# Performance work log

Measured on AMD Instinct MI355X. Metric: run time of the kernel, lower is better.

The kernel has to match this reference:

```python
import jax, jax.numpy as jnp
import numpy as np

T, H, W_, CIN, LAT, HID, OUT, NHL = 32, 64, 64, 3, 256, 256, 3, 3
OMEGA = 30.0  # SIREN sine frequency


def _uniform(key, shape, fan_in):
    b = np.sqrt(6.0 / fan_in) / OMEGA
    return jax.random.uniform(key, shape, jnp.float32, -b, b)


def setup_inputs() -> dict:
    key = jax.random.key(0)
    ks = jax.random.split(key, 10)
    return {
        "coords": jax.random.normal(ks[0], (T, H, W_, CIN), jnp.float32),
        "latents": jax.random.normal(ks[1], (T, LAT), jnp.float32),
        # shared SIREN weights (nf_net): W stored as (out, in) like nn.Linear
        "W0": _uniform(ks[2], (HID, CIN), CIN),
        "b0": jnp.zeros((HID,), jnp.float32),
        "Wh": _uniform(ks[3], (NHL, HID, HID), HID),
        "bh": jnp.zeros((NHL, HID), jnp.float32),
        "Wf": _uniform(ks[4], (OUT, HID), HID),
        "bf": jnp.zeros((OUT,), jnp.float32),
        # hypernet weight generators (hw_net), no bias
        "HW0": _uniform(ks[5], (HID * CIN, LAT), LAT),
        "HWh": _uniform(ks[6], (NHL, HID * HID, LAT), LAT),
        # hypernet bias generators (hb_net), no bias
        "HB": _uniform(ks[7], (NHL + 1, HID, LAT), LAT),
    }


def reference(coords, latents, W0, b0, Wh, bh, Wf, bf, HW0, HWh, HB):
    t = latents.shape[0]
    # per-frame hyper biases for all layers: (t, NHL+1, HID)
    hb = jnp.einsum('tl,khl->tkh', latents, HB)
    # layer 0: per-frame weight (t, HID, CIN)
    hw0 = (latents @ HW0.T).reshape(t, HID, CIN)
    x = coords  # (t,h,w,CIN)
    x = (x @ W0.T + b0
         + jnp.einsum('thwi,toi->thwo', x, hw0)
         + hb[:, 0][:, None, None, :])
    x = jnp.sin(OMEGA * x)
    for i in range(NHL):
        hw = (latents @ HWh[i].T).reshape(t, HID, HID)  # (t, HID, HID)
        x = (x @ Wh[i].T + bh[i]
             + jnp.einsum('thwi,toi->thwo', x, hw)
             + hb[:, i + 1][:, None, None, :])
        x = jnp.sin(OMEGA * x)
    return x @ Wf.T + bf  # (t,h,w,OUT)
```

## Files before the change

kernel.cpp:

```cpp
#include <hip/hip_runtime.h>
#include <cstdint>
#include <cstddef>

typedef __attribute__((ext_vector_type(8))) _Float16 f16x8;
typedef __attribute__((ext_vector_type(2))) __fp16 h2;
typedef __attribute__((ext_vector_type(16))) float f32x16;

#define LO_SCALE 2048.0f
#define LO_INV   (1.0f / 2048.0f)
#define OMEGA_SC 4.774648292756860f

union H8 { f16x8 v; _Float16 h[8]; };
union U2 { h2 v[2]; uint2 u; };

__global__ __launch_bounds__(256) void kab(
    const float* __restrict__ latents, const float* __restrict__ W0,
    const float* __restrict__ b0, const float* __restrict__ bh,
    const float* __restrict__ HW0, const float* __restrict__ HB,
    const float* __restrict__ Wh, const float* __restrict__ HWh,
    _Float16* __restrict__ w0blob, float* __restrict__ beff,
    _Float16* __restrict__ whblob) {
  __shared__ float lat_t[8192];
  int tid = threadIdx.x, bid = blockIdx.x;

  if (bid >= 768) {
    int id = (bid - 768) * 256 + tid;
    if (id < 32768) {
      int t = id >> 10, rem = id & 1023;
      int r2 = rem & 127, part = r2 >> 6, lane = r2 & 63;
      int nf = rem >> 7;
      int o = nf * 32 + (lane & 31), kc = lane >> 5;
      const float* lat = latents + t * 256;
      H8 outv;
#pragma unroll
      for (int j = 0; j < 8; ++j) outv.h[j] = (_Float16)0.0f;
#pragma unroll
      for (int j = 0; j < 8; ++j) {
        int i = kc * 8 + j;
        if (i < 3) {
          const float* row = HW0 + (o * 3 + i) * 256;
          float s = W0[o * 3 + i];
          for (int k = 0; k < 256; k += 4)
            s += row[k] * lat[k] + row[k + 1] * lat[k + 1] +
                 row[k + 2] * lat[k + 2] + row[k + 3] * lat[k + 3];
          s *= OMEGA_SC;
          _Float16 hi = (_Float16)s;
          outv.h[j] = part ? (_Float16)((s - (float)hi) * LO_SCALE) : hi;
        }
      }
      *(f16x8*)(w0blob + (size_t)id * 8) = outv.v;
    } else {
      int v = id - 32768;
      int t = v >> 10, k = (v >> 8) & 3, hm = v & 255;
      float base = (k == 0) ? b0[hm] : bh[(k - 1) * 256 + hm];
      const float* lat = latents + t * 256;
      const float* row = HB + (size_t)(k * 256 + hm) * 256;
      float s = base;
      for (int kk = 0; kk < 256; kk += 4)
        s += row[kk] * lat[kk] + row[kk + 1] * lat[kk + 1] +
             row[kk + 2] * lat[kk + 2] + row[kk + 3] * lat[kk + 3];
      beff[v] = s * OMEGA_SC;
    }
    return;
  }

  int h = bid & 1, ks = (bid >> 1) & 15, nf = (bid >> 5) & 7, l = bid >> 8;

  {
    int f = tid >> 3, kb = (tid & 7) * 32;
#pragma unroll
    for (int m = 0; m < 32; m += 4) {
      float4 v = *(const float4*)(latents + f * 256 + kb + m);
      lat_t[(kb + m + 0) * 32 + f] = v.x;
      lat_t[(kb + m + 1) * 32 + f] = v.y;
      lat_t[(kb + m + 2) * 32 + f] = v.z;
      lat_t[(kb + m + 3) * 32 + f] = v.w;
    }
  }
  __syncthreads();

  int oo = tid >> 3, jj = tid & 7;
  int o = nf * 32 + oo;
  int i = ks * 16 + h * 8 + jj;
  int r = o * 256 + i;
  const float* rowp = HWh + ((size_t)l * 65536 + (size_t)r) * 256;

  float acc[32];
#pragma unroll
  for (int f = 0; f < 32; ++f) acc[f] = 0.f;

  float curf[16], nxtf[16];
#pragma unroll
  for (int q = 0; q < 4; ++q)
    *(float4*)(curf + q * 4) = *(const float4*)(rowp + q * 4);

  for (int kc = 0; kc < 16; ++kc) {
    if (kc < 15) {
#pragma unroll
      for (int q = 0; q < 4; ++q)
        *(float4*)(nxtf + q * 4) = *(const float4*)(rowp + (kc + 1) * 16 + q * 4);
    }
    const float* lp = lat_t + kc * 512;
#pragma unroll
    for (int m = 0; m < 16; ++m) {
      float hw = curf[m];
#pragma unroll
      for (int fq = 0; fq < 8; ++fq) {
        float4 lv = *(const float4*)(lp + m * 32 + fq * 4);
        acc[fq * 4 + 0] += hw * lv.x;
        acc[fq * 4 + 1] += hw * lv.y;
        acc[fq * 4 + 2] += hw * lv.z;
        acc[fq * 4 + 3] += hw * lv.w;
      }
    }
#pragma unroll
    for (int q = 0; q < 16; ++q) curf[q] = nxtf[q];
  }

  float whv = Wh[l * 65536 + r];
  size_t cbase = (size_t)(nf * 16 + ks) * 1024 + (size_t)h * 256 + (size_t)tid;
#pragma unroll
  for (int t = 0; t < 32; ++t) {
    float w = (acc[t] + whv) * OMEGA_SC;
    _Float16 hi = (_Float16)w;
    _Float16 lo = (_Float16)((w - (float)hi) * LO_SCALE);
    size_t b = (size_t)(t * 3 + l) * 131072 + cbase;
    whblob[b] = hi;
    whblob[b + 512] = lo;
  }
}

__global__ __launch_bounds__(256, 2) void kb_siren(
    const float* __restrict__ coords, const _Float16* __restrict__ whblob,
    const _Float16* __restrict__ w0blob, const float* __restrict__ beff,
    const float* __restrict__ Wf, const float* __restrict__ bf,
    float* __restrict__ out) {
  __shared__ _Float16 xs_hi[64 * 264];
  __shared__ _Float16 xs_lo[64 * 264];
  __shared__ float wf_s[768];
  __shared__ float red[768];
  int tid = threadIdx.x;
  int bid0 = blockIdx.x;
  int bid = (bid0 & 7) * 256 + (bid0 >> 3);
  int t = bid >> 6, tile = bid & 63;
  int wv = tid >> 6, lane = tid & 63, col = lane & 31, h = lane >> 5;

  if (tid < 192) *(float4*)(wf_s + tid * 4) = *(const float4*)(Wf + tid * 4);
  if (tid < 64) {
    const float* cp = coords + (size_t)(t * 4096 + tile * 64 + tid) * 3;
    float c0 = cp[0], c1 = cp[1], c2 = cp[2];
    H8 hv, lv, z;
#pragma unroll
    for (int j = 0; j < 8; ++j) { hv.h[j] = (_Float16)0.f; lv.h[j] = (_Float16)0.f; z.h[j] = (_Float16)0.f; }
    _Float16 h0 = (_Float16)c0, h1 = (_Float16)c1, h2_ = (_Float16)c2;
    hv.h[0] = h0; hv.h[1] = h1; hv.h[2] = h2_;
    lv.h[0] = (_Float16)((c0 - (float)h0) * LO_SCALE);
    lv.h[1] = (_Float16)((c1 - (float)h1) * LO_SCALE);
    lv.h[2] = (_Float16)((c2 - (float)h2_) * LO_SCALE);
    *(f16x8*)(xs_hi + tid * 264) = hv.v;
    *(f16x8*)(xs_lo + tid * 264) = lv.v;
    *(f16x8*)(xs_hi + tid * 264 + 8) = z.v;
    *(f16x8*)(xs_lo + tid * 264 + 8) = z.v;
  }
  __syncthreads();

  f32x16 accA[2][2], accB[2][2];

  auto init_bias = [&](int bk) {
#pragma unroll
    for (int fr = 0; fr < 2; ++fr) {
      const float* bp = beff + ((t * 4 + bk) << 8) + (wv * 2 + fr) * 32 + h * 4;
#pragma unroll
      for (int rq = 0; rq < 4; ++rq) {
        float4 bvv = *(const float4*)(bp + rq * 8);
        float ba[4];
        *(float4*)ba = bvv;
#pragma unroll
        for (int q = 0; q < 4; ++q) {
          accA[fr][0][rq * 4 + q] = ba[q];
          accA[fr][1][rq * 4 + q] = ba[q];
          accB[fr][0][rq * 4 + q] = 0.f;
          accB[fr][1][rq * 4 + q] = 0.f;
        }
      }
    }
  };

  auto aload4 = [&](const _Float16* blobL, int NS, int ks,
                    f16x8& a0h, f16x8& a0l, f16x8& a1h, f16x8& a1l) {
    const _Float16* p0 = blobL + (size_t)(((wv * 2 + 0) * NS + ks) * 2) * 512 + lane * 8;
    const _Float16* p1 = blobL + (size_t)(((wv * 2 + 1) * NS + ks) * 2) * 512 + lane * 8;
    a0h = *(const f16x8*)p0;
    a0l = *(const f16x8*)(p0 + 512);
    a1h = *(const f16x8*)p1;
    a1l = *(const f16x8*)(p1 + 512);
  };

  auto mfma_step = [&](f16x8 a0h, f16x8 a0l, f16x8 a1h, f16x8 a1l, int ks) {
#pragma unroll
    for (int pf = 0; pf < 2; ++pf) {
      int off = (pf * 32 + col) * 264 + ks * 16 + h * 8;
      f16x8 bh_ = *(const f16x8*)(xs_hi + off);
      f16x8 bl_ = *(const f16x8*)(xs_lo + off);
      accA[0][pf] = __builtin_amdgcn_mfma_f32_32x32x16_f16(a0h, bh_, accA[0][pf], 0, 0, 0);
      accB[0][pf] = __builtin_amdgcn_mfma_f32_32x32x16_f16(a0h, bl_, accB[0][pf], 0, 0, 0);
      accB[0][pf] = __builtin_amdgcn_mfma_f32_32x32x16_f16(a0l, bh_, accB[0][pf], 0, 0, 0);
      accA[1][pf] = __builtin_amdgcn_mfma_f32_32x32x16_f16(a1h, bh_, accA[1][pf], 0, 0, 0);
      accB[1][pf] = __builtin_amdgcn_mfma_f32_32x32x16_f16(a1h, bl_, accB[1][pf], 0, 0, 0);
      accB[1][pf] = __builtin_amdgcn_mfma_f32_32x32x16_f16(a1l, bh_, accB[1][pf], 0, 0, 0);
    }
  };

  auto sin2pi = [](float x) {
    float f, r;
    asm("v_fract_f32 %0, %1" : "=v"(f) : "v"(x));
    asm("v_sin_f32 %0, %1" : "=v"(r) : "v"(f));
    return r;
  };

  auto epilogue = [&]() {
#pragma unroll
    for (int fr = 0; fr < 2; ++fr)
#pragma unroll
      for (int pf = 0; pf < 2; ++pf)
#pragma unroll
        for (int r = 0; r < 16; ++r)
          accA[fr][pf][r] = sin2pi(fmaf(accB[fr][pf][r], LO_INV, accA[fr][pf][r]));
    __syncthreads();
#pragma unroll
    for (int fr = 0; fr < 2; ++fr)
#pragma unroll
      for (int pf = 0; pf < 2; ++pf) {
        int base = (pf * 32 + col) * 264 + wv * 64 + fr * 32 + h * 4;
#pragma unroll
        for (int qd = 0; qd < 4; ++qd) {
          float v0 = accA[fr][pf][qd * 4 + 0];
          float v1 = accA[fr][pf][qd * 4 + 1];
          float v2 = accA[fr][pf][qd * 4 + 2];
          float v3 = accA[fr][pf][qd * 4 + 3];
          h2 ha = __builtin_amdgcn_cvt_pkrtz(v0, v1);
          h2 hb = __builtin_amdgcn_cvt_pkrtz(v2, v3);
          float l0 = (v0 - (float)ha[0]) * LO_SCALE;
          float l1 = (v1 - (float)ha[1]) * LO_SCALE;
          float l2 = (v2 - (float)hb[0]) * LO_SCALE;
          float l3 = (v3 - (float)hb[1]) * LO_SCALE;
          h2 la = __builtin_amdgcn_cvt_pkrtz(l0, l1);
          h2 lb = __builtin_amdgcn_cvt_pkrtz(l2, l3);
          U2 uh, ul;
          uh.v[0] = ha; uh.v[1] = hb;
          ul.v[0] = la; ul.v[1] = lb;
          int off = base + qd * 8;
          *(uint2*)(xs_hi + off) = uh.u;
          *(uint2*)(xs_lo + off) = ul.u;
        }
      }
    __syncthreads();
  };

  const _Float16* bl0 = whblob + (size_t)(t * 3) * 131072;
  f16x8 c0h, c0l, c1h, c1l, n0h, n0l, n1h, n1l;

  init_bias(0);
  aload4(w0blob + (size_t)t * 8192, 1, 0, c0h, c0l, c1h, c1l);
  mfma_step(c0h, c0l, c1h, c1l, 0);
  aload4(bl0, 16, 0, c0h, c0l, c1h, c1l);
  epilogue();

#pragma unroll
  for (int li = 0; li < 3; ++li) {
    init_bias(li + 1);
    const _Float16* bl = whblob + (size_t)(t * 3 + li) * 131072;
    const _Float16* bln = whblob + (size_t)(t * 3 + li + 1) * 131072;
#pragma unroll
    for (int ks2 = 0; ks2 < 8; ++ks2) {
      int ksA = ks2 * 2, ksB = ks2 * 2 + 1;
      aload4(bl, 16, ksB, n0h, n0l, n1h, n1l);
      mfma_step(c0h, c0l, c1h, c1l, ksA);
      if (ksB < 15) {
        aload4(bl, 16, ksB + 1, c0h, c0l, c1h, c1l);
      } else if (li < 2) {
        aload4(bln, 16, 0, c0h, c0l, c1h, c1l);
      }
      mfma_step(n0h, n0l, n1h, n1l, ksB);
    }
    epilogue();
  }

  {
    float pc0 = 0.f, pc1 = 0.f, pc2 = 0.f;
    int px = tid & 63, kq = tid >> 6;
#pragma unroll
    for (int cc = 0; cc < 8; ++cc) {
      int k0 = kq * 64 + cc * 8;
      H8 hv, lv;
      hv.v = *(const f16x8*)(xs_hi + px * 264 + k0);
      lv.v = *(const f16x8*)(xs_lo + px * 264 + k0);
#pragma unroll
      for (int j = 0; j < 8; ++j) {
        float xv = (float)hv.h[j] + (float)lv.h[j] * LO_INV;
        pc0 += xv * wf_s[k0 + j];
        pc1 += xv * wf_s[256 + k0 + j];
        pc2 += xv * wf_s[512 + k0 + j];
      }
    }
    red[kq * 192 + px * 3 + 0] = pc0;
    red[kq * 192 + px * 3 + 1] = pc1;
    red[kq * 192 + px * 3 + 2] = pc2;
    __syncthreads();
    if (tid < 192) {
      int p2 = tid / 3, c = tid - p2 * 3;
      float s = bf[c];
#pragma unroll
      for (int q = 0; q < 4; ++q) s += red[q * 192 + p2 * 3 + c];
      out[(size_t)(t * 4096 + tile * 64 + p2) * 3 + c] = s;
    }
  }
}

extern "C" void kernel_launch(void* const* d_in, const int* in_sizes, int n_in,
                              void* d_out, int out_size, void* d_ws, size_t ws_size,
                              hipStream_t stream) {
  const float* coords  = (const float*)d_in[0];
  const float* latents = (const float*)d_in[1];
  const float* W0      = (const float*)d_in[2];
  const float* b0      = (const float*)d_in[3];
  const float* Wh      = (const float*)d_in[4];
  const float* bh      = (const float*)d_in[5];
  const float* Wf      = (const float*)d_in[6];
  const float* bf      = (const float*)d_in[7];
  const float* HW0     = (const float*)d_in[8];
  const float* HWh     = (const float*)d_in[9];
  const float* HB      = (const float*)d_in[10];
  float* outp = (float*)d_out;

  char* w = (char*)d_ws;
  _Float16* whblob = (_Float16*)w;
  _Float16* w0blob = (_Float16*)(w + 25165824);
  float*    beff   = (float*)(w + 25690112);

  kab<<<1024, 256, 0, stream>>>(latents, W0, b0, bh, HW0, HB, Wh, HWh,
                                w0blob, beff, whblob);
  kb_siren<<<2048, 256, 0, stream>>>(coords, whblob, w0blob, beff, Wf, bf, outp);
}
```

Measured before the change: 216.3 us.

## Permute K layout for vectorized LDS stores and software-pipeline B-fragment loads

Permutes the K (input-feature) ordering of the generated hypernet weights, the layer-0 weights and the Wf staging so that each lane's MFMA output maps onto contiguous 16 halves. The epilogue can then write 128-bit LDS stores instead of 64-bit ones. B fragments are now double-buffered in registers and prefetched one k-step ahead, and the 12 MFMAs are reordered to interleave independent accumulators under s_setprio. The goal is to cut LDS store count and hide LDS read latency behind MFMA issue, at the cost of more VGPR pressure under launch_bounds(256,2).

```diff
diff --git a/kernel.cpp b/kernel.cpp
--- a/kernel.cpp
+++ b/kernel.cpp
@@ -11,7 +11,8 @@
 #define OMEGA_SC 4.774648292756860f
 
 union H8 { f16x8 v; _Float16 h[8]; };
-union U2 { h2 v[2]; uint2 u; };
+union HU { f16x8 v; h2 p[4]; };
+
 
 __global__ __launch_bounds__(256) void kab(
     const float* __restrict__ latents, const float* __restrict__ W0,
@@ -36,7 +37,7 @@
       for (int j = 0; j < 8; ++j) outv.h[j] = (_Float16)0.0f;
 #pragma unroll
       for (int j = 0; j < 8; ++j) {
-        int i = kc * 8 + j;
+        int i = (j & 3) + 8 * (j >> 2) + 16 * kc;
         if (i < 3) {
           const float* row = HW0 + (o * 3 + i) * 256;
           float s = W0[o * 3 + i];
@@ -81,7 +82,7 @@
 
   int oo = tid >> 3, jj = tid & 7;
   int o = nf * 32 + oo;
-  int i = ks * 16 + h * 8 + jj;
+  int i = (ks >> 1) * 32 + (ks & 1) * 4 + (jj & 3) + 8 * ((jj >> 2) & 1) + 16 * h;
   int r = o * 256 + i;
   const float* rowp = HWh + ((size_t)l * 65536 + (size_t)r) * 256;
 
@@ -145,7 +146,13 @@
   int t = bid >> 6, tile = bid & 63;
   int wv = tid >> 6, lane = tid & 63, col = lane & 31, h = lane >> 5;
 
-  if (tid < 192) *(float4*)(wf_s + tid * 4) = *(const float4*)(Wf + tid * 4);
+  if (tid < 192) {
+    int c = tid >> 6;
+    int pq = (tid & 63) * 4;
+    int blk = pq >> 5, p32 = pq & 31, hq = p32 >> 4, rr = p32 & 15;
+    int src = c * 256 + blk * 32 + 8 * (rr >> 2) + 4 * hq;
+    *(float4*)(wf_s + tid * 4) = *(const float4*)(Wf + src);
+  }
   if (tid < 64) {
     const float* cp = coords + (size_t)(t * 4096 + tile * 64 + tid) * 3;
     float c0 = cp[0], c1 = cp[1], c2 = cp[2];
@@ -196,19 +203,31 @@
     a1l = *(const f16x8*)(p1 + 512);
   };
 
-  auto mfma_step = [&](f16x8 a0h, f16x8 a0l, f16x8 a1h, f16x8 a1l, int ks) {
-#pragma unroll
-    for (int pf = 0; pf < 2; ++pf) {
-      int off = (pf * 32 + col) * 264 + ks * 16 + h * 8;
-      f16x8 bh_ = *(const f16x8*)(xs_hi + off);
-      f16x8 bl_ = *(const f16x8*)(xs_lo + off);
-      accA[0][pf] = __builtin_amdgcn_mfma_f32_32x32x16_f16(a0h, bh_, accA[0][pf], 0, 0, 0);
-      accB[0][pf] = __builtin_amdgcn_mfma_f32_32x32x16_f16(a0h, bl_, accB[0][pf], 0, 0, 0);
-      accB[0][pf] = __builtin_amdgcn_mfma_f32_32x32x16_f16(a0l, bh_, accB[0][pf], 0, 0, 0);
-      accA[1][pf] = __builtin_amdgcn_mfma_f32_32x32x16_f16(a1h, bh_, accA[1][pf], 0, 0, 0);
-      accB[1][pf] = __builtin_amdgcn_mfma_f32_32x32x16_f16(a1h, bl_, accB[1][pf], 0, 0, 0);
-      accB[1][pf] = __builtin_amdgcn_mfma_f32_32x32x16_f16(a1l, bh_, accB[1][pf], 0, 0, 0);
-    }
+  auto bload = [&](int ks, f16x8& b0h, f16x8& b0l, f16x8& b1h, f16x8& b1l) {
+    int off0 = col * 264 + ks * 16 + h * 8;
+    int off1 = (32 + col) * 264 + ks * 16 + h * 8;
+    b0h = *(const f16x8*)(xs_hi + off0);
+    b0l = *(const f16x8*)(xs_lo + off0);
+    b1h = *(const f16x8*)(xs_hi + off1);
+    b1l = *(const f16x8*)(xs_lo + off1);
+  };
+
+  auto mfma12 = [&](f16x8 a0h, f16x8 a0l, f16x8 a1h, f16x8 a1l,
+                    f16x8 b0h, f16x8 b0l, f16x8 b1h, f16x8 b1l) {
+    __builtin_amdgcn_s_setprio(1);
+    accA[0][0] = __builtin_amdgcn_mfma_f32_32x32x16_f16(a0h, b0h, accA[0][0], 0, 0, 0);
+    accA[1][0] = __builtin_amdgcn_mfma_f32_32x32x16_f16(a1h, b0h, accA[1][0], 0, 0, 0);
+    accA[0][1] = __builtin_amdgcn_mfma_f32_32x32x16_f16(a0h, b1h, accA[0][1], 0, 0, 0);
+    accA[1][1] = __builtin_amdgcn_mfma_f32_32x32x16_f16(a1h, b1h, accA[1][1], 0, 0, 0);
+    accB[0][0] = __builtin_amdgcn_mfma_f32_32x32x16_f16(a0h, b0l, accB[0][0], 0, 0, 0);
+    accB[1][0] = __builtin_amdgcn_mfma_f32_32x32x16_f16(a1h, b0l, accB[1][0], 0, 0, 0);
+    accB[0][1] = __builtin_amdgcn_mfma_f32_32x32x16_f16(a0h, b1l, accB[0][1], 0, 0, 0);
+    accB[1][1] = __builtin_amdgcn_mfma_f32_32x32x16_f16(a1h, b1l, accB[1][1], 0, 0, 0);
+    accB[0][0] = __builtin_amdgcn_mfma_f32_32x32x16_f16(a0l, b0h, accB[0][0], 0, 0, 0);
+    accB[1][0] = __builtin_amdgcn_mfma_f32_32x32x16_f16(a1l, b0h, accB[1][0], 0, 0, 0);
+    accB[0][1] = __builtin_amdgcn_mfma_f32_32x32x16_f16(a0l, b1h, accB[0][1], 0, 0, 0);
+    accB[1][1] = __builtin_amdgcn_mfma_f32_32x32x16_f16(a1l, b1h, accB[1][1], 0, 0, 0);
+    __builtin_amdgcn_s_setprio(0);
   };
 
   auto sin2pi = [](float x) {
@@ -231,38 +250,37 @@
     for (int fr = 0; fr < 2; ++fr)
 #pragma unroll
       for (int pf = 0; pf < 2; ++pf) {
-        int base = (pf * 32 + col) * 264 + wv * 64 + fr * 32 + h * 4;
-#pragma unroll
-        for (int qd = 0; qd < 4; ++qd) {
-          float v0 = accA[fr][pf][qd * 4 + 0];
-          float v1 = accA[fr][pf][qd * 4 + 1];
-          float v2 = accA[fr][pf][qd * 4 + 2];
-          float v3 = accA[fr][pf][qd * 4 + 3];
-          h2 ha = __builtin_amdgcn_cvt_pkrtz(v0, v1);
-          h2 hb = __builtin_amdgcn_cvt_pkrtz(v2, v3);
-          float l0 = (v0 - (float)ha[0]) * LO_SCALE;
-          float l1 = (v1 - (float)ha[1]) * LO_SCALE;
-          float l2 = (v2 - (float)hb[0]) * LO_SCALE;
-          float l3 = (v3 - (float)hb[1]) * LO_SCALE;
-          h2 la = __builtin_amdgcn_cvt_pkrtz(l0, l1);
-          h2 lb = __builtin_amdgcn_cvt_pkrtz(l2, l3);
-          U2 uh, ul;
-          uh.v[0] = ha; uh.v[1] = hb;
-          ul.v[0] = la; ul.v[1] = lb;
-          int off = base + qd * 8;
-          *(uint2*)(xs_hi + off) = uh.u;
-          *(uint2*)(xs_lo + off) = ul.u;
+        HU h0, h1, l0, l1;
+#pragma unroll
+        for (int q = 0; q < 4; ++q) {
+          float va = accA[fr][pf][2 * q], vb = accA[fr][pf][2 * q + 1];
+          h2 hp = __builtin_amdgcn_cvt_pkrtz(va, vb);
+          h0.p[q] = hp;
+          l0.p[q] = __builtin_amdgcn_cvt_pkrtz((va - (float)hp[0]) * LO_SCALE,
+                                               (vb - (float)hp[1]) * LO_SCALE);
+          float vc = accA[fr][pf][8 + 2 * q], vd = accA[fr][pf][8 + 2 * q + 1];
+          h2 hq_ = __builtin_amdgcn_cvt_pkrtz(vc, vd);
+          h1.p[q] = hq_;
+          l1.p[q] = __builtin_amdgcn_cvt_pkrtz((vc - (float)hq_[0]) * LO_SCALE,
+                                               (vd - (float)hq_[1]) * LO_SCALE);
         }
+        int off = (pf * 32 + col) * 264 + wv * 64 + fr * 32 + h * 16;
+        *(f16x8*)(xs_hi + off) = h0.v;
+        *(f16x8*)(xs_hi + off + 8) = h1.v;
+        *(f16x8*)(xs_lo + off) = l0.v;
+        *(f16x8*)(xs_lo + off + 8) = l1.v;
       }
     __syncthreads();
   };
 
   const _Float16* bl0 = whblob + (size_t)(t * 3) * 131072;
   f16x8 c0h, c0l, c1h, c1l, n0h, n0l, n1h, n1l;
+  f16x8 cb0h, cb0l, cb1h, cb1l, nb0h, nb0l, nb1h, nb1l;
 
   init_bias(0);
   aload4(w0blob + (size_t)t * 8192, 1, 0, c0h, c0l, c1h, c1l);
-  mfma_step(c0h, c0l, c1h, c1l, 0);
+  bload(0, cb0h, cb0l, cb1h, cb1l);
+  mfma12(c0h, c0l, c1h, c1l, cb0h, cb0l, cb1h, cb1l);
   aload4(bl0, 16, 0, c0h, c0l, c1h, c1l);
   epilogue();
 
@@ -271,17 +289,20 @@
     init_bias(li + 1);
     const _Float16* bl = whblob + (size_t)(t * 3 + li) * 131072;
     const _Float16* bln = whblob + (size_t)(t * 3 + li + 1) * 131072;
+    bload(0, cb0h, cb0l, cb1h, cb1l);
 #pragma unroll
     for (int ks2 = 0; ks2 < 8; ++ks2) {
-      int ksA = ks2 * 2, ksB = ks2 * 2 + 1;
+      int ksB = ks2 * 2 + 1;
+      bload(ksB, nb0h, nb0l, nb1h, nb1l);
       aload4(bl, 16, ksB, n0h, n0l, n1h, n1l);
-      mfma_step(c0h, c0l, c1h, c1l, ksA);
+      mfma12(c0h, c0l, c1h, c1l, cb0h, cb0l, cb1h, cb1l);
       if (ksB < 15) {
+        bload(ksB + 1, cb0h, cb0l, cb1h, cb1l);
         aload4(bl, 16, ksB + 1, c0h, c0l, c1h, c1l);
       } else if (li < 2) {
         aload4(bln, 16, 0, c0h, c0l, c1h, c1l);
       }
-      mfma_step(n0h, n0l, n1h, n1l, ksB);
+      mfma12(n0h, n0l, n1h, n1l, nb0h, nb0l, nb1h, nb1l);
     }
     epilogue();
   }
```

New measurement: 231.3 us. +7.0%, slower.
